# Kernel optimization log

Measured on AMD Instinct MI355X. Metric: run time of the kernel, lower is better.

The kernel has to match this reference:

```python
import jax, jax.numpy as jnp
import numpy as np

TOPK_FRAC = 0.9
LEAKY_SLOPE = 0.01
BN_EPS = 1e-5


def setup_inputs() -> dict:
    key = jax.random.key(0)
    k1, k2 = jax.random.split(key)
    B, C_in, N, C_out = 8, 256, 2048, 256
    x = jax.random.normal(k1, (B, C_in, N), dtype=jnp.float32)
    stdv = 1.0 / np.sqrt(C_out)
    weight = jax.random.uniform(k2, (C_in, C_out), dtype=jnp.float32, minval=-stdv, maxval=stdv)
    bn_weight = jnp.zeros((C_out,), dtype=jnp.float32)
    bn_bias = jnp.zeros((C_out,), dtype=jnp.float32)
    return {"x": x, "weight": weight, "bn_weight": bn_weight, "bn_bias": bn_bias}


def _norm_adj(xn):
    # xn: [B, N, C]
    adj = jax.nn.softmax(jnp.einsum('bnc,bmc->bnm', xn, xn), axis=-1)  # [B,N,N]
    N = adj.shape[1]
    k = int(round(N * TOPK_FRAC))
    topv, _ = jax.lax.top_k(adj, k)                     # [B,N,k]
    thresh = topv[..., -1:]                              # k-th largest per row
    return jnp.where(adj >= thresh, adj, 0.0)           # keep top-k, zero rest


def reference(x, weight, bn_weight, bn_bias):
    # x: [B, C_in, N] -> [B, N, C_in]
    xn = jnp.transpose(x, (0, 2, 1))
    adj = _norm_adj(xn)                                  # [B,N,N]
    support = jnp.einsum('bnc,cd->bnd', xn, weight)      # [B,N,C_out]
    out = jnp.einsum('bnm,bmd->bnd', adj, support)       # [B,N,C_out]
    out = jnp.transpose(out, (0, 2, 1))                  # [B,C_out,N]
    out = jnp.where(out >= 0, out, LEAKY_SLOPE * out)    # LeakyReLU
    # BatchNorm1d (training-mode batch stats) over (B, N) per channel
    mean = jnp.mean(out, axis=(0, 2), keepdims=True)
    var = jnp.mean(jnp.square(out - mean), axis=(0, 2), keepdims=True)
    out = (out - mean) * jax.lax.rsqrt(var + BN_EPS)
    return out * bn_weight[None, :, None] + bn_bias[None, :, None]
```

## Files before the change

### kernel.cpp

```cpp
#include <hip/hip_runtime.h>

#define B_ 8
#define C_ 256
#define N_ 2048
#define D_ 256
#define KKEEP 1843
#define LEAKY 0.01f
#define EPS 1e-5f

using short8  = __attribute__((ext_vector_type(8))) short;
using ushort8 = __attribute__((ext_vector_type(8))) unsigned short;
using ushort4v = __attribute__((ext_vector_type(4))) unsigned short;
using f32x4   = __attribute__((ext_vector_type(4))) float;

__device__ inline unsigned short f2bf(float x) {
  unsigned u = __float_as_uint(x);
  u += 0x7fffu + ((u >> 16) & 1u);
  return (unsigned short)(u >> 16);
}
__device__ inline float bf2f(unsigned short u) { return __uint_as_float(((unsigned)u) << 16); }

__global__ __launch_bounds__(256) void k_transpose_cast(const float* __restrict__ src,
                                                        unsigned short* __restrict__ dst,
                                                        int rows, int cols,
                                                        size_t srcBatch, size_t dstBatch) {
  __shared__ float tile[32][33];
  int b = blockIdx.z;
  src += (size_t)b * srcBatch;
  dst += (size_t)b * dstBatch;
  int i0 = blockIdx.y * 32;
  int j0 = blockIdx.x * 32;
  int t = threadIdx.x;
  int tc = t & 31, tr = t >> 5;
#pragma unroll
  for (int k = 0; k < 4; ++k)
    tile[tr + k * 8][tc] = src[(size_t)(i0 + tr + k * 8) * cols + j0 + tc];
  __syncthreads();
  int r2 = t >> 3, q = t & 7;
  ushort4v v;
#pragma unroll
  for (int l = 0; l < 4; ++l) v[l] = f2bf(tile[q * 4 + l][r2]);
  *(ushort4v*)&dst[(size_t)(j0 + r2) * rows + i0 + q * 4] = v;
}

template<int K_, int BN, bool OUT_BF16, bool DO_LEAKY, bool SWZ>
__global__ __launch_bounds__(256) void k_gemm(const short* __restrict__ A,
                                              const short* __restrict__ Bt,
                                              void* __restrict__ Cout,
                                              size_t aStride, size_t bStride, size_t cStride,
                                              int ldc, int nx) {
  constexpr int FI = (BN == 128) ? 4 : 2;
  __shared__ short As[128][44];
  __shared__ short Bs[BN][44];
  int b, bxi, byi;
  if constexpr (SWZ) {
    int lin = blockIdx.x;
    b = lin & 7;
    int rest = lin >> 3;
    bxi = rest % nx;
    byi = rest / nx;
  } else {
    b = blockIdx.z; bxi = blockIdx.x; byi = blockIdx.y;
  }
  A += (size_t)b * aStride;
  Bt += (size_t)b * bStride;
  int bi = byi * 128;
  int bj = bxi * BN;
  int t = threadIdx.x;
  int lane = t & 63, wid = t >> 6;
  int wr, wc;
  if constexpr (BN == 128) { wr = (wid >> 1) * 64; wc = (wid & 1) * 64; }
  else                     { wr = wid * 32;        wc = 0; }

  int r0 = t >> 2, k0 = (t & 3) * 8;
  int r1 = r0 + 64;
  const short* aP0 = A + (size_t)(bi + r0) * K_ + k0;
  const short* aP1 = A + (size_t)(bi + r1) * K_ + k0;
  const short* bP0 = Bt + (size_t)(bj + r0) * K_ + k0;
  const short* bP1 = Bt + (size_t)(bj + (BN == 128 ? r1 : r0)) * K_ + k0;

  short8 a0 = *(const short8*)aP0;
  short8 a1 = *(const short8*)aP1;
  short8 b0 = *(const short8*)bP0;
  short8 b1;
  if constexpr (BN == 128) b1 = *(const short8*)bP1;

  f32x4 acc[FI][4];
  f32x4 z = {0.f, 0.f, 0.f, 0.f};
#pragma unroll
  for (int i = 0; i < FI; ++i)
#pragma unroll
    for (int j = 0; j < 4; ++j) acc[i][j] = z;

  int fr = lane & 15;
  int ks = (lane >> 4) * 8;

  for (int c0 = 0; c0 < K_; c0 += 32) {
    __syncthreads();
    *(short8*)&As[r0][k0] = a0;
    *(short8*)&As[r1][k0] = a1;
    *(short8*)&Bs[r0][k0] = b0;
    if constexpr (BN == 128) *(short8*)&Bs[r1][k0] = b1;
    __syncthreads();
    if (c0 + 32 < K_) {
      a0 = *(const short8*)(aP0 + c0 + 32);
      a1 = *(const short8*)(aP1 + c0 + 32);
      b0 = *(const short8*)(bP0 + c0 + 32);
      if constexpr (BN == 128) b1 = *(const short8*)(bP1 + c0 + 32);
    }
    short8 af[FI], bf[4];
#pragma unroll
    for (int f = 0; f < FI; ++f) af[f] = *(const short8*)&As[wr + f * 16 + fr][ks];
#pragma unroll
    for (int f = 0; f < 4; ++f)  bf[f] = *(const short8*)&Bs[wc + f * 16 + fr][ks];
#pragma unroll
    for (int fi = 0; fi < FI; ++fi)
#pragma unroll
      for (int fj = 0; fj < 4; ++fj)
        acc[fi][fj] = __builtin_amdgcn_mfma_f32_16x16x32_bf16(af[fi], bf[fj], acc[fi][fj], 0, 0, 0);
  }

  int orow = (lane >> 4) * 4;
  int ocol = lane & 15;
#pragma unroll
  for (int fi = 0; fi < FI; ++fi)
#pragma unroll
    for (int fj = 0; fj < 4; ++fj)
#pragma unroll
      for (int r = 0; r < 4; ++r) {
        float v = acc[fi][fj][r];
        if (DO_LEAKY) v = (v >= 0.f) ? v : LEAKY * v;
        size_t idx = (size_t)b * cStride +
                     (size_t)(bi + wr + fi * 16 + orow + r) * ldc +
                     (size_t)(bj + wc + fj * 16 + ocol);
        if (OUT_BF16) ((unsigned short*)Cout)[idx] = f2bf(v);
        else          ((float*)Cout)[idx] = v;
      }
}

__global__ __launch_bounds__(256) void k_softmax_topk(unsigned short* __restrict__ S) {
  int t = threadIdx.x;
  int lane = t & 63, wv = t >> 6;
  size_t row = (size_t)blockIdx.x * 4 + wv;
  unsigned short* sr = S + row * N_;

  float e[32];
#pragma unroll
  for (int i = 0; i < 4; ++i) {
    ushort8 raw = *(const ushort8*)(sr + ((size_t)(i * 64 + lane)) * 8);
#pragma unroll
    for (int j = 0; j < 8; ++j) e[i * 8 + j] = bf2f(raw[j]);
  }

  float lm = e[0];
#pragma unroll
  for (int j = 1; j < 32; ++j) lm = fmaxf(lm, e[j]);
#pragma unroll
  for (int m = 1; m <= 16; m <<= 1) lm = fmaxf(lm, __shfl_xor(lm, m));
  lm = fmaxf(__shfl(lm, 0), __shfl(lm, 32));

  float ls = 0.f;
#pragma unroll
  for (int j = 0; j < 32; ++j) { e[j] = __expf(e[j] - lm); ls += e[j]; }
#pragma unroll
  for (int m = 1; m <= 16; m <<= 1) ls += __shfl_xor(ls, m);
  ls = __shfl(ls, 0) + __shfl(ls, 32);
  float inv = 1.0f / ls;

  unsigned kp[16], vo[16];
#pragma unroll
  for (int q = 0; q < 16; ++q)
    kp[q] = (unsigned)f2bf(e[q]) | ((unsigned)f2bf(e[q + 16]) << 16);
#pragma unroll
  for (int q = 0; q < 16; ++q)
    vo[q] = (unsigned)f2bf(e[2 * q] * inv) | ((unsigned)f2bf(e[2 * q + 1] * inv) << 16);

  unsigned tp[16];
#pragma unroll
  for (int q = 0; q < 16; ++q) tp[q] = kp[q];
#pragma unroll
  for (int sI = 0; sI < 4; ++sI) {
    const int s = 8 >> sI;
    const unsigned msk = (s == 8) ? 0x00FF00FFu : (s == 4) ? 0x0F0F0F0Fu
                       : (s == 2) ? 0x33333333u : 0x55555555u;
#pragma unroll
    for (int k = 0; k < 16; ++k) {
      if ((k & s) == 0) {
        unsigned tt = ((tp[k] >> s) ^ tp[k + s]) & msk;
        tp[k + s] ^= tt;
        tp[k]     ^= tt << s;
      }
    }
  }

  unsigned alive = 0xFFFFFFFFu, prefix = 0u;
  int need = KKEEP;
#pragma unroll
  for (int b = 12; b >= 0; b -= 2) {
    unsigned p1 = tp[b + 1], p0 = tp[b];
    unsigned hi = alive & p1;
    unsigned m3 = hi & p0, m2 = hi & ~p0, m1v = (alive & ~p1) & p0;
    unsigned packed = (unsigned)__popc(m3) | ((unsigned)__popc(m2) << 11) |
                      ((unsigned)__popc(m1v) << 22);
#pragma unroll
    for (int m = 1; m <= 16; m <<= 1) packed += __shfl_xor(packed, m);
    unsigned v0 = __shfl(packed, 0), v32 = __shfl(packed, 32);
    int C3 = (int)((v0 & 0x7FFu) + (v32 & 0x7FFu));
    int C2 = (int)(((v0 >> 11) & 0x7FFu) + ((v32 >> 11) & 0x7FFu));
    int C1 = (int)(((v0 >> 22) & 0x7FFu) + ((v32 >> 22) & 0x7FFu));
    int cum2 = C3 + C2, cum1 = cum2 + C1;
    if (C3 >= need)        { alive = m3;  prefix |= 3u << b; }
    else if (cum2 >= need) { alive = m2;  prefix |= 2u << b; need -= C3; }
    else if (cum1 >= need) { alive = m1v; prefix |= 1u << b; need -= cum2; }
    else                   { alive ^= (m3 | m2 | m1v);       need -= cum1; }
  }

#pragma unroll
  for (int i = 0; i < 4; ++i) {
    ushort8 o;
#pragma unroll
    for (int j = 0; j < 8; ++j) {
      int idx = i * 8 + j;
      unsigned key = (kp[idx & 15] >> ((idx >> 4) * 16)) & 0xFFFFu;
      unsigned val = (vo[idx >> 1] >> ((idx & 1) * 16)) & 0xFFFFu;
      o[j] = (key >= prefix) ? (unsigned short)val : (unsigned short)0;
    }
    *(ushort8*)(sr + ((size_t)(i * 64 + lane)) * 8) = o;
  }
}

__global__ __launch_bounds__(256) void k_stats(const float* __restrict__ pre,
                                               float* __restrict__ ps,
                                               float* __restrict__ pss) {
  int t = threadIdx.x;
  int g = blockIdx.x;
  const int ROWS = (B_ * N_) / 256;
  const float* pb = pre + (size_t)g * ROWS * D_;
  float s = 0.f, ss = 0.f;
  for (int r = 0; r < ROWS; ++r) {
    float vv = pb[(size_t)r * D_ + t];
    s += vv;
    ss = fmaf(vv, vv, ss);
  }
  ps[g * 256 + t] = s;
  pss[g * 256 + t] = ss;
}

__global__ void k_final(const float* __restrict__ ps, const float* __restrict__ pss,
                        const float* __restrict__ bnw, const float* __restrict__ bnb,
                        float* __restrict__ scale, float* __restrict__ shift) {
  int t = threadIdx.x;
  float s = 0.f, ss = 0.f;
  for (int g = 0; g < 256; ++g) {
    s += ps[g * 256 + t];
    ss += pss[g * 256 + t];
  }
  const float invN = 1.0f / (B_ * N_);
  float mean = s * invN;
  float var = fmaf(-mean, mean, ss * invN);
  float istd = rsqrtf(var + EPS);
  float sc = istd * bnw[t];
  scale[t] = sc;
  shift[t] = fmaf(-mean, sc, bnb[t]);
}

__global__ __launch_bounds__(256) void k_out(const float* __restrict__ pre,
                                             const float* __restrict__ scale,
                                             const float* __restrict__ shift,
                                             float* __restrict__ out) {
  __shared__ float tile[32][33];
  int blk = blockIdx.x;
  int d0 = (blk % (D_ / 32)) * 32;
  int n0 = ((blk / (D_ / 32)) % (N_ / 32)) * 32;
  int b = blk / ((D_ / 32) * (N_ / 32));
  int tc = threadIdx.x & 31;
  int tr = threadIdx.x >> 5;
  const float* pb = pre + ((size_t)b * N_ + n0) * D_ + d0;
#pragma unroll
  for (int i = 0; i < 4; ++i) {
    int r = tr + i * 8;
    tile[r][tc] = pb[(size_t)r * D_ + tc];
  }
  __syncthreads();
  float* ob = out + ((size_t)b * D_ + d0) * N_ + n0;
#pragma unroll
  for (int i = 0; i < 4; ++i) {
    int r = tr + i * 8;
    float vv = tile[tc][r];
    ob[(size_t)r * N_ + tc] = fmaf(vv, scale[d0 + r], shift[d0 + r]);
  }
}

extern "C" void kernel_launch(void* const* d_in, const int* in_sizes, int n_in,
                              void* d_out, int out_size, void* d_ws, size_t ws_size,
                              hipStream_t stream) {
  const float* x = (const float*)d_in[0];
  const float* W = (const float*)d_in[1];
  const float* bnw = (const float*)d_in[2];
  const float* bnb = (const float*)d_in[3];
  float* out = (float*)d_out;

  char* w = (char*)d_ws;
  short* xt = (short*)w;            w += (size_t)B_ * N_ * C_ * 2;
  short* wt = (short*)w;            w += (size_t)D_ * C_ * 2;
  short* supT = (short*)w;          w += (size_t)B_ * D_ * N_ * 2;
  short* S = (short*)w;             w += (size_t)B_ * N_ * N_ * 2;
  float* pre = (float*)w;           w += (size_t)B_ * N_ * D_ * 4;
  float* ps = (float*)w;            w += 256 * 256 * 4;
  float* pss = (float*)w;           w += 256 * 256 * 4;
  float* scale = (float*)w;         w += D_ * 4;
  float* shift = (float*)w;         w += D_ * 4;

  k_transpose_cast<<<dim3(N_ / 32, C_ / 32, B_), 256, 0, stream>>>(
      x, (unsigned short*)xt, C_, N_, (size_t)C_ * N_, (size_t)N_ * C_);
  k_transpose_cast<<<dim3(D_ / 32, C_ / 32, 1), 256, 0, stream>>>(
      W, (unsigned short*)wt, C_, D_, 0, 0);

  k_gemm<C_, 64, true, false, false><<<dim3(N_ / 64, 2, B_), 256, 0, stream>>>(
      wt, xt, supT, 0, (size_t)N_ * C_, (size_t)D_ * N_, N_, 0);

  k_gemm<C_, 128, true, false, true><<<dim3(16 * 16 * B_, 1, 1), 256, 0, stream>>>(
      xt, xt, S, (size_t)N_ * C_, (size_t)N_ * C_, (size_t)N_ * N_, N_, 16);

  k_softmax_topk<<<B_ * N_ / 4, 256, 0, stream>>>((unsigned short*)S);

  k_gemm<N_, 64, false, true, true><<<dim3(4 * 16 * B_, 1, 1), 256, 0, stream>>>(
      S, supT, pre, (size_t)N_ * N_, (size_t)D_ * N_, (size_t)N_ * D_, D_, 4);

  k_stats<<<256, 256, 0, stream>>>(pre, ps, pss);
  k_final<<<1, 256, 0, stream>>>(ps, pss, bnw, bnb, scale, shift);
  k_out<<<B_ * (N_ / 32) * (D_ / 32), 256, 0, stream>>>(pre, scale, shift, out);
}
```

Before: 131.9 us.

## Fuse softmax/top-k masking into adj@support GEMM and fold BN stats into epilogue

The softmax+top-k kernel becomes a read-only row-stats pass that stores max, inverse sum and a score threshold per row. A new GEMM recomputes exp and applies the mask while staging A tiles into shared memory, so the masked probability matrix is never written back. The GEMM epilogue applies LeakyReLU, writes the pre-activation in bf16, and emits per-block channel sums, which removes the separate stats kernel. The cost is redoing exp for each output-column block (four times per element) and a somewhat different masking rule (comparing scores instead of bf16 keys), which could keep tied values differently.

```diff
diff --git a/kernel.cpp b/kernel.cpp
--- a/kernel.cpp
+++ b/kernel.cpp
@@ -7,6 +7,7 @@
 #define KKEEP 1843
 #define LEAKY 0.01f
 #define EPS 1e-5f
+#define L2E 1.4426950408889634f
 
 using short8  = __attribute__((ext_vector_type(8))) short;
 using ushort8 = __attribute__((ext_vector_type(8))) unsigned short;
@@ -43,10 +44,10 @@
   *(ushort4v*)&dst[(size_t)(j0 + r2) * rows + i0 + q * 4] = v;
 }
 
-template<int K_, int BN, bool OUT_BF16, bool DO_LEAKY, bool SWZ>
+template<int K_, int BN, bool SWZ>
 __global__ __launch_bounds__(256) void k_gemm(const short* __restrict__ A,
                                               const short* __restrict__ Bt,
-                                              void* __restrict__ Cout,
+                                              unsigned short* __restrict__ Cout,
                                               size_t aStride, size_t bStride, size_t cStride,
                                               int ldc, int nx) {
   constexpr int FI = (BN == 128) ? 4 : 2;
@@ -128,52 +129,48 @@
     for (int fj = 0; fj < 4; ++fj)
 #pragma unroll
       for (int r = 0; r < 4; ++r) {
-        float v = acc[fi][fj][r];
-        if (DO_LEAKY) v = (v >= 0.f) ? v : LEAKY * v;
         size_t idx = (size_t)b * cStride +
                      (size_t)(bi + wr + fi * 16 + orow + r) * ldc +
                      (size_t)(bj + wc + fj * 16 + ocol);
-        if (OUT_BF16) ((unsigned short*)Cout)[idx] = f2bf(v);
-        else          ((float*)Cout)[idx] = v;
+        Cout[idx] = f2bf(acc[fi][fj][r]);
       }
 }
 
-__global__ __launch_bounds__(256) void k_softmax_topk(unsigned short* __restrict__ S) {
+__global__ __launch_bounds__(256) void k_rowstats(const unsigned short* __restrict__ S,
+                                                  float4* __restrict__ rowp) {
   int t = threadIdx.x;
   int lane = t & 63, wv = t >> 6;
   size_t row = (size_t)blockIdx.x * 4 + wv;
-  unsigned short* sr = S + row * N_;
-
-  float e[32];
+  const unsigned short* sr = S + row * N_;
+
+  float sc[32];
 #pragma unroll
   for (int i = 0; i < 4; ++i) {
     ushort8 raw = *(const ushort8*)(sr + ((size_t)(i * 64 + lane)) * 8);
 #pragma unroll
-    for (int j = 0; j < 8; ++j) e[i * 8 + j] = bf2f(raw[j]);
-  }
-
-  float lm = e[0];
-#pragma unroll
-  for (int j = 1; j < 32; ++j) lm = fmaxf(lm, e[j]);
+    for (int j = 0; j < 8; ++j) sc[i * 8 + j] = bf2f(raw[j]);
+  }
+
+  float lm = sc[0];
+#pragma unroll
+  for (int j = 1; j < 32; ++j) lm = fmaxf(lm, sc[j]);
 #pragma unroll
   for (int m = 1; m <= 16; m <<= 1) lm = fmaxf(lm, __shfl_xor(lm, m));
   lm = fmaxf(__shfl(lm, 0), __shfl(lm, 32));
+  float nm = -lm * L2E;
 
   float ls = 0.f;
-#pragma unroll
-  for (int j = 0; j < 32; ++j) { e[j] = __expf(e[j] - lm); ls += e[j]; }
+  unsigned kp[16];
+#pragma unroll
+  for (int q = 0; q < 16; ++q) {
+    float ea = exp2f(fmaf(sc[q], L2E, nm));
+    float eb = exp2f(fmaf(sc[q + 16], L2E, nm));
+    ls += ea + eb;
+    kp[q] = (unsigned)f2bf(ea) | ((unsigned)f2bf(eb) << 16);
+  }
 #pragma unroll
   for (int m = 1; m <= 16; m <<= 1) ls += __shfl_xor(ls, m);
   ls = __shfl(ls, 0) + __shfl(ls, 32);
-  float inv = 1.0f / ls;
-
-  unsigned kp[16], vo[16];
-#pragma unroll
-  for (int q = 0; q < 16; ++q)
-    kp[q] = (unsigned)f2bf(e[q]) | ((unsigned)f2bf(e[q + 16]) << 16);
-#pragma unroll
-  for (int q = 0; q < 16; ++q)
-    vo[q] = (unsigned)f2bf(e[2 * q] * inv) | ((unsigned)f2bf(e[2 * q + 1] * inv) << 16);
 
   unsigned tp[16];
 #pragma unroll
@@ -215,46 +212,152 @@
     else                   { alive ^= (m3 | m2 | m1v);       need -= cum1; }
   }
 
-#pragma unroll
-  for (int i = 0; i < 4; ++i) {
-    ushort8 o;
-#pragma unroll
-    for (int j = 0; j < 8; ++j) {
-      int idx = i * 8 + j;
-      unsigned key = (kp[idx & 15] >> ((idx >> 4) * 16)) & 0xFFFFu;
-      unsigned val = (vo[idx >> 1] >> ((idx & 1) * 16)) & 0xFFFFu;
-      o[j] = (key >= prefix) ? (unsigned short)val : (unsigned short)0;
-    }
-    *(ushort8*)(sr + ((size_t)(i * 64 + lane)) * 8) = o;
-  }
-}
-
-__global__ __launch_bounds__(256) void k_stats(const float* __restrict__ pre,
-                                               float* __restrict__ ps,
-                                               float* __restrict__ pss) {
-  int t = threadIdx.x;
-  int g = blockIdx.x;
-  const int ROWS = (B_ * N_) / 256;
-  const float* pb = pre + (size_t)g * ROWS * D_;
-  float s = 0.f, ss = 0.f;
-  for (int r = 0; r < ROWS; ++r) {
-    float vv = pb[(size_t)r * D_ + t];
-    s += vv;
-    ss = fmaf(vv, vv, ss);
-  }
-  ps[g * 256 + t] = s;
-  pss[g * 256 + t] = ss;
+  float thr = 1e30f;
+#pragma unroll
+  for (int j = 0; j < 32; ++j) {
+    unsigned key = (kp[j & 15] >> ((j >> 4) * 16)) & 0xFFFFu;
+    if (key >= prefix) thr = fminf(thr, sc[j]);
+  }
+#pragma unroll
+  for (int m = 1; m <= 16; m <<= 1) thr = fminf(thr, __shfl_xor(thr, m));
+  thr = fminf(__shfl(thr, 0), __shfl(thr, 32));
+
+  if (lane == 0) rowp[row] = make_float4(nm, 1.0f / ls, thr, 0.f);
+}
+
+__device__ inline short8 cvt_mask(short8 raw, float nm, float iv, float thr) {
+  short8 o;
+#pragma unroll
+  for (int j = 0; j < 8; ++j) {
+    float s = bf2f((unsigned short)raw[j]);
+    float e = exp2f(fmaf(s, L2E, nm));
+    float p = (s >= thr) ? e * iv : 0.f;
+    o[j] = (short)f2bf(p);
+  }
+  return o;
+}
+
+__global__ __launch_bounds__(256) void k_pv(const short* __restrict__ A,
+                                            const short* __restrict__ Bt,
+                                            const float4* __restrict__ rowp,
+                                            unsigned short* __restrict__ pre,
+                                            float* __restrict__ ps, float* __restrict__ pss) {
+  __shared__ short As[128][44];
+  __shared__ short Bs[64][44];
+  int lin = blockIdx.x;
+  int b = lin & 7;
+  int rest = lin >> 3;
+  int bxi = rest & 3;
+  int byi = rest >> 2;
+  const short* Ab = A + (size_t)b * N_ * N_;
+  const short* Bb = Bt + (size_t)b * D_ * N_;
+  int bi = byi * 128, bj = bxi * 64;
+  int t = threadIdx.x, lane = t & 63, wid = t >> 6;
+  int wr = wid * 32;
+
+  int r0 = t >> 2, k0 = (t & 3) * 8;
+  int r1 = r0 + 64;
+  const short* aP0 = Ab + (size_t)(bi + r0) * N_ + k0;
+  const short* aP1 = Ab + (size_t)(bi + r1) * N_ + k0;
+  const short* bP0 = Bb + (size_t)(bj + r0) * N_ + k0;
+
+  float4 rp0 = rowp[(size_t)b * N_ + bi + r0];
+  float4 rp1 = rowp[(size_t)b * N_ + bi + r1];
+
+  short8 a0 = *(const short8*)aP0;
+  short8 a1 = *(const short8*)aP1;
+  short8 b0 = *(const short8*)bP0;
+
+  f32x4 acc[2][4];
+  f32x4 z = {0.f, 0.f, 0.f, 0.f};
+#pragma unroll
+  for (int i = 0; i < 2; ++i)
+#pragma unroll
+    for (int j = 0; j < 4; ++j) acc[i][j] = z;
+
+  int fr = lane & 15;
+  int ks = (lane >> 4) * 8;
+
+  for (int c0 = 0; c0 < N_; c0 += 32) {
+    __syncthreads();
+    *(short8*)&As[r0][k0] = cvt_mask(a0, rp0.x, rp0.y, rp0.z);
+    *(short8*)&As[r1][k0] = cvt_mask(a1, rp1.x, rp1.y, rp1.z);
+    *(short8*)&Bs[r0][k0] = b0;
+    __syncthreads();
+    if (c0 + 32 < N_) {
+      a0 = *(const short8*)(aP0 + c0 + 32);
+      a1 = *(const short8*)(aP1 + c0 + 32);
+      b0 = *(const short8*)(bP0 + c0 + 32);
+    }
+    short8 af[2], bf[4];
+#pragma unroll
+    for (int f = 0; f < 2; ++f) af[f] = *(const short8*)&As[wr + f * 16 + fr][ks];
+#pragma unroll
+    for (int f = 0; f < 4; ++f) bf[f] = *(const short8*)&Bs[f * 16 + fr][ks];
+#pragma unroll
+    for (int fi = 0; fi < 2; ++fi)
+#pragma unroll
+      for (int fj = 0; fj < 4; ++fj)
+        acc[fi][fj] = __builtin_amdgcn_mfma_f32_16x16x32_bf16(af[fi], bf[fj], acc[fi][fj], 0, 0, 0);
+  }
+
+  int orow = (lane >> 4) * 4;
+  int ocol = lane & 15;
+  float s4[4] = {0.f, 0.f, 0.f, 0.f}, ss4[4] = {0.f, 0.f, 0.f, 0.f};
+#pragma unroll
+  for (int fi = 0; fi < 2; ++fi)
+#pragma unroll
+    for (int r = 0; r < 4; ++r) {
+      int rowg = bi + wr + fi * 16 + orow + r;
+      size_t base = ((size_t)b * N_ + rowg) * D_ + bj;
+#pragma unroll
+      for (int fj = 0; fj < 4; ++fj) {
+        float v = acc[fi][fj][r];
+        v = (v >= 0.f) ? v : LEAKY * v;
+        pre[base + fj * 16 + ocol] = f2bf(v);
+        s4[fj] += v;
+        ss4[fj] = fmaf(v, v, ss4[fj]);
+      }
+    }
+#pragma unroll
+  for (int fj = 0; fj < 4; ++fj) {
+    s4[fj] += __shfl_xor(s4[fj], 16);  s4[fj] += __shfl_xor(s4[fj], 32);
+    ss4[fj] += __shfl_xor(ss4[fj], 16); ss4[fj] += __shfl_xor(ss4[fj], 32);
+  }
+  __syncthreads();
+  float* sred = (float*)As;
+  if (lane < 16) {
+#pragma unroll
+    for (int fj = 0; fj < 4; ++fj) {
+      sred[(wid * 4 + fj) * 16 + lane] = s4[fj];
+      sred[256 + (wid * 4 + fj) * 16 + lane] = ss4[fj];
+    }
+  }
+  __syncthreads();
+  if (t < 64) {
+    float s = 0.f, ss = 0.f;
+#pragma unroll
+    for (int w4 = 0; w4 < 4; ++w4) {
+      s  += sred[(w4 * 4 + (t >> 4)) * 16 + (t & 15)];
+      ss += sred[256 + (w4 * 4 + (t >> 4)) * 16 + (t & 15)];
+    }
+    ps[(size_t)lin * 64 + t] = s;
+    pss[(size_t)lin * 64 + t] = ss;
+  }
 }
 
 __global__ void k_final(const float* __restrict__ ps, const float* __restrict__ pss,
                         const float* __restrict__ bnw, const float* __restrict__ bnb,
                         float* __restrict__ scale, float* __restrict__ shift) {
   int t = threadIdx.x;
+  int bxi = t >> 6, col = t & 63;
   float s = 0.f, ss = 0.f;
-  for (int g = 0; g < 256; ++g) {
-    s += ps[g * 256 + t];
-    ss += pss[g * 256 + t];
-  }
+  for (int byi = 0; byi < 16; ++byi)
+    for (int bb = 0; bb < 8; ++bb) {
+      int lin = (byi * 4 + bxi) * 8 + bb;
+      s += ps[(size_t)lin * 64 + col];
+      ss += pss[(size_t)lin * 64 + col];
+    }
   const float invN = 1.0f / (B_ * N_);
   float mean = s * invN;
   float var = fmaf(-mean, mean, ss * invN);
@@ -264,7 +367,7 @@
   shift[t] = fmaf(-mean, sc, bnb[t]);
 }
 
-__global__ __launch_bounds__(256) void k_out(const float* __restrict__ pre,
+__global__ __launch_bounds__(256) void k_out(const unsigned short* __restrict__ pre,
                                              const float* __restrict__ scale,
                                              const float* __restrict__ shift,
                                              float* __restrict__ out) {
@@ -275,11 +378,11 @@
   int b = blk / ((D_ / 32) * (N_ / 32));
   int tc = threadIdx.x & 31;
   int tr = threadIdx.x >> 5;
-  const float* pb = pre + ((size_t)b * N_ + n0) * D_ + d0;
+  const unsigned short* pb = pre + ((size_t)b * N_ + n0) * D_ + d0;
 #pragma unroll
   for (int i = 0; i < 4; ++i) {
     int r = tr + i * 8;
-    tile[r][tc] = pb[(size_t)r * D_ + tc];
+    tile[r][tc] = bf2f(pb[(size_t)r * D_ + tc]);
   }
   __syncthreads();
   float* ob = out + ((size_t)b * D_ + d0) * N_ + n0;
@@ -305,9 +408,10 @@
   short* wt = (short*)w;            w += (size_t)D_ * C_ * 2;
   short* supT = (short*)w;          w += (size_t)B_ * D_ * N_ * 2;
   short* S = (short*)w;             w += (size_t)B_ * N_ * N_ * 2;
-  float* pre = (float*)w;           w += (size_t)B_ * N_ * D_ * 4;
-  float* ps = (float*)w;            w += 256 * 256 * 4;
-  float* pss = (float*)w;           w += 256 * 256 * 4;
+  unsigned short* pre = (unsigned short*)w; w += (size_t)B_ * N_ * D_ * 2;
+  float4* rowp = (float4*)w;        w += (size_t)B_ * N_ * 16;
+  float* ps = (float*)w;            w += (size_t)512 * 64 * 4;
+  float* pss = (float*)w;           w += (size_t)512 * 64 * 4;
   float* scale = (float*)w;         w += D_ * 4;
   float* shift = (float*)w;         w += D_ * 4;
 
@@ -316,18 +420,17 @@
   k_transpose_cast<<<dim3(D_ / 32, C_ / 32, 1), 256, 0, stream>>>(
       W, (unsigned short*)wt, C_, D_, 0, 0);
 
-  k_gemm<C_, 64, true, false, false><<<dim3(N_ / 64, 2, B_), 256, 0, stream>>>(
-      wt, xt, supT, 0, (size_t)N_ * C_, (size_t)D_ * N_, N_, 0);
-
-  k_gemm<C_, 128, true, false, true><<<dim3(16 * 16 * B_, 1, 1), 256, 0, stream>>>(
-      xt, xt, S, (size_t)N_ * C_, (size_t)N_ * C_, (size_t)N_ * N_, N_, 16);
-
-  k_softmax_topk<<<B_ * N_ / 4, 256, 0, stream>>>((unsigned short*)S);
-
-  k_gemm<N_, 64, false, true, true><<<dim3(4 * 16 * B_, 1, 1), 256, 0, stream>>>(
-      S, supT, pre, (size_t)N_ * N_, (size_t)D_ * N_, (size_t)N_ * D_, D_, 4);
-
-  k_stats<<<256, 256, 0, stream>>>(pre, ps, pss);
+  k_gemm<C_, 64, false><<<dim3(N_ / 64, 2, B_), 256, 0, stream>>>(
+      wt, xt, (unsigned short*)supT, 0, (size_t)N_ * C_, (size_t)D_ * N_, N_, 0);
+
+  k_gemm<C_, 128, true><<<dim3(16 * 16 * B_, 1, 1), 256, 0, stream>>>(
+      xt, xt, (unsigned short*)S, (size_t)N_ * C_, (size_t)N_ * C_, (size_t)N_ * N_, N_, 16);
+
+  k_rowstats<<<B_ * N_ / 4, 256, 0, stream>>>((unsigned short*)S, rowp);
+
+  k_pv<<<dim3(4 * 16 * B_, 1, 1), 256, 0, stream>>>(
+      S, supT, rowp, pre, ps, pss);
+
   k_final<<<1, 256, 0, stream>>>(ps, pss, bnw, bnb, scale, shift);
   k_out<<<B_ * (N_ / 32) * (D_ / 32), 256, 0, stream>>>(pre, scale, shift, out);
 }
```

After: 172.5 us. 1.31x slower.
